# Optimization experiments

Hardware: AMD Instinct MI355X
Metric: run time of the kernel (lower is better)

The kernel has to match this reference:

```python
import jax, jax.numpy as jnp
import numpy as np

PLANES, RATIO = 512, 4
Q = PLANES // RATIO  # 128
B, H, W = 4, 128, 128


def _dw_stride2(x, k):
    # depthwise 3x3 stride-2 conv, NCHW, kernel [C,1,3,3]
    return jax.lax.conv_general_dilated(
        x, k, window_strides=(2, 2), padding=((1, 1), (1, 1)),
        feature_group_count=x.shape[1],
        dimension_numbers=('NCHW', 'OIHW', 'NCHW'))


def _upsample_bilinear_ac(x, out_h, out_w):
    # bilinear, align_corners=True (matches F.interpolate)
    n, c, h, w = x.shape
    def co(out, ins):
        s = (ins - 1) / (out - 1)
        pos = jnp.arange(out, dtype=jnp.float32) * jnp.float32(s)
        i0 = jnp.floor(pos).astype(jnp.int32)
        i1 = jnp.minimum(i0 + 1, ins - 1)
        return i0, i1, pos - i0.astype(jnp.float32)
    y0, y1, ty = co(out_h, h)
    x0, x1, tx = co(out_w, w)
    rows = x[:, :, y0, :] * (1 - ty)[None, None, :, None] + x[:, :, y1, :] * ty[None, None, :, None]
    return rows[:, :, :, x0] * (1 - tx) + rows[:, :, :, x1] * tx


def setup_inputs() -> dict:
    key = jax.random.key(0)
    ks = jax.random.split(key, 32)
    nrm = lambda k, s, sc=0.05: jax.random.normal(k, s, jnp.float32) * sc
    uni = lambda k, s: jax.random.uniform(k, s, jnp.float32, 0.5, 1.5)
    return {
        'feat': jax.random.normal(ks[0], (B, PLANES, H, W), jnp.float32),
        'w_phi': nrm(ks[1], (2 * Q, PLANES)),
        'bn_phi_s': uni(ks[2], (2 * Q,)), 'bn_phi_b': nrm(ks[3], (2 * Q,)),
        'w_theta': nrm(ks[4], (Q, PLANES)),
        'bn_theta_s': uni(ks[5], (Q,)), 'bn_theta_b': nrm(ks[6], (Q,)),
        'w_adj': nrm(ks[7], (Q, Q)),
        'bn_adj_s': uni(ks[8], (Q,)), 'bn_adj_b': nrm(ks[9], (Q,)),
        'w_wg': nrm(ks[10], (2 * Q, 2 * Q)),
        'bn_wg_s': uni(ks[11], (2 * Q,)), 'bn_wg_b': nrm(ks[12], (2 * Q,)),
        'w_conv3': nrm(ks[13], (PLANES, 2 * Q)),
        'bn3_s': uni(ks[14], (PLANES,)), 'bn3_b': nrm(ks[15], (PLANES,)),
        'w_local1': nrm(ks[16], (PLANES, 1, 3, 3), 0.2),
        'bnl1_s': uni(ks[17], (PLANES,)), 'bnl1_b': nrm(ks[18], (PLANES,)),
        'w_local2': nrm(ks[19], (PLANES, 1, 3, 3), 0.2),
        'bnl2_s': uni(ks[20], (PLANES,)), 'bnl2_b': nrm(ks[21], (PLANES,)),
        'w_local3': nrm(ks[22], (PLANES, 1, 3, 3), 0.2),
        'bnl3_s': uni(ks[23], (PLANES,)), 'bnl3_b': nrm(ks[24], (PLANES,)),
        'gamma': nrm(ks[25], (1,), 0.5),
        'w_final': nrm(ks[26], (PLANES, 2 * PLANES)),
        'bnf_s': uni(ks[27], (PLANES,)), 'bnf_b': nrm(ks[28], (PLANES,)),
    }


def reference(feat, w_phi, bn_phi_s, bn_phi_b, w_theta, bn_theta_s, bn_theta_b,
              w_adj, bn_adj_s, bn_adj_b, w_wg, bn_wg_s, bn_wg_b,
              w_conv3, bn3_s, bn3_b,
              w_local1, bnl1_s, bnl1_b, w_local2, bnl2_s, bnl2_b,
              w_local3, bnl3_s, bnl3_b, gamma, w_final, bnf_s, bnf_b):
    n, c, h, w = feat.shape
    bn2 = lambda x, s, b: x * s[None, :, None, None] + b[None, :, None, None]
    bn1 = lambda x, s, b: x * s[None, :, None] + b[None, :, None]
    conv1x1 = lambda x, wt: jnp.einsum('oc,nchw->nohw', wt, x)

    l = bn2(_dw_stride2(feat, w_local1), bnl1_s, bnl1_b)
    l = bn2(_dw_stride2(l, w_local2), bnl2_s, bnl2_b)
    l = bn2(_dw_stride2(l, w_local3), bnl3_s, bnl3_b)
    nl, cl, hl, wl = l.shape
    v = l.reshape(nl, cl, hl * wl)                      # [n,C,hw]
    energy = jnp.einsum('nck,ndk->ncd', v, v)           # [n,C,C]
    attn = jax.nn.softmax(jnp.max(energy, -1, keepdims=True) - energy, axis=-1)
    cam = jnp.einsum('ncd,ndk->nck', attn, v).reshape(nl, cl, hl, wl)
    l = gamma * cam + l
    local = _upsample_bilinear_ac(l, h, w)
    spatial_local_feat = feat * local + feat

    # ---- graph branch
    q = w_theta.shape[0]
    x_sqz = bn2(conv1x1(feat, w_phi), bn_phi_s, bn_phi_b).reshape(n, 2 * q, h * w)
    b_m = bn2(conv1x1(feat, w_theta), bn_theta_s, bn_theta_b).reshape(n, q, h * w)
    z_idt = jnp.einsum('nck,ndk->ncd', x_sqz, b_m)      # [n,2q,q]
    z = jnp.swapaxes(z_idt, 1, 2)                       # [n,q,2q]
    z = bn1(jnp.einsum('oi,nil->nol', w_adj, z), bn_adj_s, bn_adj_b)
    z = jnp.swapaxes(z, 1, 2) + z_idt                   # [n,2q,q]
    z = bn1(jnp.einsum('oi,nil->nol', w_wg, z), bn_wg_s, bn_wg_b)
    y = jnp.einsum('ncd,ndk->nck', z, b_m).reshape(n, 2 * q, h, w)
    y = bn2(conv1x1(y, w_conv3), bn3_s, bn3_b)
    g_out = jax.nn.relu(feat + y)

    out = bn2(conv1x1(jnp.concatenate([spatial_local_feat, g_out], axis=1), w_final), bnf_s, bnf_b)
    return out
```

## Files before the change

### kernel.cpp

```cpp
#include <hip/hip_runtime.h>
#include <hip/hip_bf16.h>
#include <cstddef>
#include <cstdint>

static constexpr int NB  = 4;
static constexpr int CH  = 512;
static constexpr int HH  = 128;
static constexpr int WWi = 128;
static constexpr int HW  = HH * WWi;
static constexpr int Qd  = 128;
static constexpr int Q2d = 256;

typedef __attribute__((ext_vector_type(8))) short bf8;
typedef __attribute__((ext_vector_type(4))) float f4;

__device__ __forceinline__ short f2bf(float x) {
  __hip_bfloat16 h = __float2bfloat16(x);
  short s; __builtin_memcpy(&s, &h, 2); return s;
}
__device__ __forceinline__ float bfs2f(short u) {
  union { unsigned int i; float f; } x;
  x.i = ((unsigned int)(unsigned short)u) << 16; return x.f;
}

__launch_bounds__(256)
__global__ void dw_conv_bn4(const float* __restrict__ in, float* __restrict__ out,
                            const float* __restrict__ wgt, const float* __restrict__ s,
                            const float* __restrict__ b, int Hi, int Wi, int Ho, int Wo4) {
  int idx = blockIdx.x * 256 + threadIdx.x;
  int q = idx % Wo4; int t = idx / Wo4;
  int ho = t % Ho; t /= Ho;
  int c = t % CH;
  const float* ip = in + (size_t)t * Hi * Wi;
  const float* wp = wgt + c * 9;
  float w[9];
#pragma unroll
  for (int k = 0; k < 9; k++) w[k] = wp[k];
  const int x0 = q * 8;
  float acc0 = 0.f, acc1 = 0.f, acc2 = 0.f, acc3 = 0.f;
#pragma unroll
  for (int kh = 0; kh < 3; kh++) {
    int y = ho * 2 - 1 + kh;
    if ((unsigned)y < (unsigned)Hi) {
      const float* row = ip + (size_t)y * Wi + x0;
      float4 v0 = *(const float4*)row;
      float4 v1 = *(const float4*)(row + 4);
      float left = (x0 > 0) ? row[-1] : 0.f;
      float xs[9] = {left, v0.x, v0.y, v0.z, v0.w, v1.x, v1.y, v1.z, v1.w};
      const float w0 = w[kh * 3 + 0], w1 = w[kh * 3 + 1], w2 = w[kh * 3 + 2];
      acc0 += w0 * xs[0] + w1 * xs[1] + w2 * xs[2];
      acc1 += w0 * xs[2] + w1 * xs[3] + w2 * xs[4];
      acc2 += w0 * xs[4] + w1 * xs[5] + w2 * xs[6];
      acc3 += w0 * xs[6] + w1 * xs[7] + w2 * xs[8];
    }
  }
  const float sc = s[c], bb = b[c];
  float4 o;
  o.x = acc0 * sc + bb; o.y = acc1 * sc + bb;
  o.z = acc2 * sc + bb; o.w = acc3 * sc + bb;
  *(float4*)(out + (size_t)idx * 4) = o;
}

__launch_bounds__(256)
__global__ void lrow_kernel(const float* __restrict__ lcam, float* __restrict__ lrow) {
  int idx = blockIdx.x * 256 + threadIdx.x;
  int wcol = idx & 127; int t = idx >> 7;
  int hy = t & 15; t >>= 4;
  float pos = wcol * (15.f / 127.f);
  int x0 = (int)pos; if (x0 > 15) x0 = 15;
  float tx = pos - x0;
  int x1 = x0 + 1; if (x1 > 15) x1 = 15;
  const float* lc = lcam + ((size_t)t * 16 + hy) * 16;
  lrow[idx] = lc[x0] * (1.f - tx) + lc[x1] * tx;
}

__launch_bounds__(256)
__global__ void cvt_f32_bf16(const float* __restrict__ in, short* __restrict__ out, int n4) {
  int i = blockIdx.x * 256 + threadIdx.x;
  if (i >= n4) return;
  float4 v = ((const float4*)in)[i];
  short tmp[4] = {f2bf(v.x), f2bf(v.y), f2bf(v.z), f2bf(v.w)};
  short4 o; __builtin_memcpy(&o, tmp, 8);
  ((short4*)out)[i] = o;
}

__device__ __forceinline__ int sls(int row, int slot) {
  return row * 64 + ((slot ^ (((row >> 1) ^ (row >> 3)) & 7)) << 3);
}

__device__ __forceinline__ void stg64_dma(const short* __restrict__ src, size_t stride,
                                          int kb, short* lds, int t) {
  const int lane = t & 63, w = t >> 6;
#pragma unroll
  for (int i2 = 0; i2 < 4; i2++) {
    int r0 = w * 32 + i2 * 8;
    int row = r0 + (lane >> 3);
    int sl = (lane & 7) ^ (((row >> 1) ^ (row >> 3)) & 7);
    const short* g = src + (size_t)row * stride + kb + sl * 8;
    short* l = lds + r0 * 64;
    __builtin_amdgcn_global_load_lds(
        (const __attribute__((address_space(1))) unsigned int*)g,
        (__attribute__((address_space(3))) unsigned int*)l, 16, 0, 0);
  }
}

__device__ __forceinline__ void stg64_b16(const short* __restrict__ src, size_t stride,
                                          int kb, short* lds, int t) {
#pragma unroll
  for (int i = 0; i < 4; i++) {
    int chunk = t + i * 256;
    int row = chunk >> 3, slot = chunk & 7;
    bf8 v = *(const bf8*)(src + (size_t)row * stride + kb + slot * 8);
    *(bf8*)(lds + sls(row, slot)) = v;
  }
}
__device__ __forceinline__ void stg64_f32(const float* __restrict__ src, size_t stride,
                                          int kb, short* lds, int t) {
#pragma unroll
  for (int i = 0; i < 4; i++) {
    int chunk = t + i * 256;
    int row = chunk >> 3, slot = chunk & 7;
    const float* sp = src + (size_t)row * stride + kb + slot * 8;
    float4 v0 = *(const float4*)sp, v1 = *(const float4*)(sp + 4);
    union { short s[8]; bf8 v; } u;
    u.s[0] = f2bf(v0.x); u.s[1] = f2bf(v0.y); u.s[2] = f2bf(v0.z); u.s[3] = f2bf(v0.w);
    u.s[4] = f2bf(v1.x); u.s[5] = f2bf(v1.y); u.s[6] = f2bf(v1.z); u.s[7] = f2bf(v1.w);
    *(bf8*)(lds + sls(row, slot)) = u.v;
  }
}
__device__ __forceinline__ void stg64_t32(const float* __restrict__ src, size_t sstride,
                                          int pb, short* lds, int t) {
#pragma unroll
  for (int i2 = 0; i2 < 4; i2++) {
    int chunk = t + i2 * 256;
    int c = (chunk >> 3) & 63;
    int p8 = ((chunk & 7) | ((chunk >> 6) & 8)) * 8;
    const float* fr = src + (size_t)c * sstride + pb + p8;
    float4 f0 = *(const float4*)fr, f1 = *(const float4*)(fr + 4);
    float fv[8];
    __builtin_memcpy(&fv[0], &f0, 16); __builtin_memcpy(&fv[4], &f1, 16);
    int slot = c >> 3, eidx = c & 7;
#pragma unroll
    for (int e = 0; e < 8; e++) {
      lds[sls(p8 + e, slot) + eidx] = f2bf(fv[e]);
    }
  }
}
__device__ __forceinline__ void stg64_t16(const short* __restrict__ src, size_t sstride,
                                          int pb, short* lds, int t) {
#pragma unroll
  for (int i2 = 0; i2 < 4; i2++) {
    int chunk = t + i2 * 256;
    int c = (chunk >> 3) & 63;
    int p8 = ((chunk & 7) | ((chunk >> 6) & 8)) * 8;
    bf8 v = *(const bf8*)(src + (size_t)c * sstride + pb + p8);
    int slot = c >> 3, eidx = c & 7;
#pragma unroll
    for (int e = 0; e < 8; e++) {
      lds[sls(p8 + e, slot) + eidx] = v[e];
    }
  }
}
__device__ __forceinline__ bf8 fragld64(const short* lds, int row, int kk, int lg) {
  return *(const bf8*)(lds + sls(row, kk * 4 + lg));
}

__launch_bounds__(256)
__global__ void slf_build_T(const float* __restrict__ feat, const float* __restrict__ lrw,
                            short* __restrict__ slfbT, int h0) {
  const int cb = blockIdx.x * 64;
  const int hh = blockIdx.y;
  const int n  = blockIdx.z;
  const int h  = hh + h0;
  const int t  = threadIdx.x;
  __shared__ __align__(16) short lT[8192];
  const float posy = h * (15.f / 127.f);
  int hy0 = (int)posy; if (hy0 > 15) hy0 = 15;
  int hy1 = hy0 + 1; if (hy1 > 15) hy1 = 15;
  const float tyv = posy - hy0;
#pragma unroll
  for (int i2 = 0; i2 < 4; i2++) {
    int chunk = t + i2 * 256;
    int c = (chunk >> 3) & 63;
    int w8 = ((chunk & 7) | ((chunk >> 6) & 8)) * 8;
    size_t cidx = (size_t)(n * CH) + cb + c;
    const float* fr = feat + cidx * HW + h * WWi + w8;
    const float* l0r = lrw + (cidx * 16 + hy0) * WWi + w8;
    const float* l1r = lrw + (cidx * 16 + hy1) * WWi + w8;
    float4 f0 = *(const float4*)fr, f1 = *(const float4*)(fr + 4);
    float4 a0 = *(const float4*)l0r, a1 = *(const float4*)(l0r + 4);
    float4 b0 = *(const float4*)l1r, b1 = *(const float4*)(l1r + 4);
    float fv[8], av[8], bv[8];
    __builtin_memcpy(&fv[0], &f0, 16); __builtin_memcpy(&fv[4], &f1, 16);
    __builtin_memcpy(&av[0], &a0, 16); __builtin_memcpy(&av[4], &a1, 16);
    __builtin_memcpy(&bv[0], &b0, 16); __builtin_memcpy(&bv[4], &b1, 16);
    int slot = c >> 3, eidx = c & 7;
#pragma unroll
    for (int e = 0; e < 8; e++) {
      float v = fv[e] * (1.f + av[e] + (bv[e] - av[e]) * tyv);
      lT[sls(w8 + e, slot) + eidx] = f2bf(v);
    }
  }
  __syncthreads();
#pragma unroll
  for (int i2 = 0; i2 < 4; i2++) {
    int chunk = t + i2 * 256;
    int w = chunk >> 3, slot = chunk & 7;
    bf8 v = *(const bf8*)(lT + sls(w, slot));
    *(bf8*)(slfbT + (((size_t)(n * 64) + hh) * WWi + w) * CH + cb + slot * 8) = v;
  }
}

__launch_bounds__(256)
__global__ void energy_mfma(const float* __restrict__ l3, float* __restrict__ energy) {
  const int c0 = blockIdx.x * 128;
  const int d0 = blockIdx.y * 128;
  const int n = blockIdx.z;
  const int t = threadIdx.x;
  const int lane16 = t & 15, lg = (t >> 4) & 3, wave = t >> 6;
  const int wm = (wave >> 1) * 64, wn = (wave & 1) * 64;
  __shared__ __align__(16) short lA[8192], lB[8192];
  const float* srcA = l3 + ((size_t)n * CH + c0) * 256;
  const float* srcB = l3 + ((size_t)n * CH + d0) * 256;
  f4 acc[4][4];
#pragma unroll
  for (int i = 0; i < 4; i++)
#pragma unroll
    for (int j = 0; j < 4; j++) acc[i][j] = (f4)0.f;
  for (int kb = 0; kb < 256; kb += 64) {
    stg64_f32(srcA, 256, kb, lA, t);
    stg64_f32(srcB, 256, kb, lB, t);
    __syncthreads();
#pragma unroll
    for (int kk = 0; kk < 2; kk++) {
      bf8 av[4], bv[4];
#pragma unroll
      for (int i = 0; i < 4; i++) av[i] = fragld64(lA, wm + i * 16 + lane16, kk, lg);
#pragma unroll
      for (int j = 0; j < 4; j++) bv[j] = fragld64(lB, wn + j * 16 + lane16, kk, lg);
#pragma unroll
      for (int i = 0; i < 4; i++)
#pragma unroll
        for (int j = 0; j < 4; j++)
          acc[i][j] = __builtin_amdgcn_mfma_f32_16x16x32_bf16(av[i], bv[j], acc[i][j], 0, 0, 0);
    }
    __syncthreads();
  }
#pragma unroll
  for (int i = 0; i < 4; i++)
#pragma unroll
    for (int j = 0; j < 4; j++) {
      int d = d0 + wn + j * 16 + lane16;
#pragma unroll
      for (int r = 0; r < 4; r++) {
        int c = c0 + wm + i * 16 + lg * 4 + r;
        energy[((size_t)n * CH + c) * CH + d] = acc[i][j][r];
      }
    }
}

__launch_bounds__(256)
__global__ void softmax_attn(float* __restrict__ energy) {
  float* row = energy + (size_t)blockIdx.x * CH;
  int t = threadIdx.x;
  __shared__ float red[256];
  float e0 = row[t], e1 = row[t + 256];
  red[t] = fminf(e0, e1);
  __syncthreads();
  for (int s = 128; s > 0; s >>= 1) {
    if (t < s) red[t] = fminf(red[t], red[t + s]);
    __syncthreads();
  }
  float emin = red[0];
  __syncthreads();
  float w0 = __expf(emin - e0), w1 = __expf(emin - e1);
  red[t] = w0 + w1;
  __syncthreads();
  for (int s = 128; s > 0; s >>= 1) {
    if (t < s) red[t] += red[t + s];
    __syncthreads();
  }
  float inv = 1.f / red[0];
  row[t] = w0 * inv;
  row[t + 256] = w1 * inv;
}

__launch_bounds__(256)
__global__ void cam_mfma(const float* __restrict__ attn, const float* __restrict__ l3,
                         const float* __restrict__ gamma, float* __restrict__ lcam) {
  const int pb = blockIdx.x * 128;
  const int mb = blockIdx.y * 128;
  const int n = blockIdx.z;
  const int t = threadIdx.x;
  const int lane16 = t & 15, lg = (t >> 4) & 3, wave = t >> 6;
  const int wm = (wave >> 1) * 64, wn = (wave & 1) * 64;
  __shared__ __align__(16) short lA[8192], lB[8192];
  const float* srcA = attn + ((size_t)n * CH + mb) * CH;
  const float gm = gamma[0];
  f4 acc[4][4];
#pragma unroll
  for (int i = 0; i < 4; i++)
#pragma unroll
    for (int j = 0; j < 4; j++) acc[i][j] = (f4)0.f;
  for (int kb = 0; kb < 512; kb += 64) {
    stg64_f32(srcA, CH, kb, lA, t);
    stg64_t32(l3 + ((size_t)n * CH + kb) * 256, 256, pb, lB, t);
    __syncthreads();
#pragma unroll
    for (int kk = 0; kk < 2; kk++) {
      bf8 av[4], bv[4];
#pragma unroll
      for (int i = 0; i < 4; i++) av[i] = fragld64(lA, wm + i * 16 + lane16, kk, lg);
#pragma unroll
      for (int j = 0; j < 4; j++) bv[j] = fragld64(lB, wn + j * 16 + lane16, kk, lg);
#pragma unroll
      for (int i = 0; i < 4; i++)
#pragma unroll
        for (int j = 0; j < 4; j++)
          acc[i][j] = __builtin_amdgcn_mfma_f32_16x16x32_bf16(av[i], bv[j], acc[i][j], 0, 0, 0);
    }
    __syncthreads();
  }
#pragma unroll
  for (int i = 0; i < 4; i++)
#pragma unroll
    for (int j = 0; j < 4; j++) {
      int p = pb + wn + j * 16 + lane16;
#pragma unroll
      for (int r = 0; r < 4; r++) {
        int c = mb + wm + i * 16 + lg * 4 + r;
        size_t idx = ((size_t)n * CH + c) * 256 + p;
        lcam[idx] = gm * acc[i][j][r] + l3[idx];
      }
    }
}

__launch_bounds__(256)
__global__ void theta_mfma2(const short* __restrict__ wthb, const float* __restrict__ feat,
                            const float* __restrict__ s, const float* __restrict__ b,
                            short* __restrict__ bmb) {
  const int pb = blockIdx.x * 128;
  const int n = blockIdx.y;
  const int t = threadIdx.x;
  const int lane16 = t & 15, lg = (t >> 4) & 3, wave = t >> 6;
  const int wm = (wave >> 1) * 64, wn = (wave & 1) * 64;
  __shared__ __align__(16) short lA[8192], lB[8192];
  f4 acc[4][4];
#pragma unroll
  for (int i = 0; i < 4; i++)
#pragma unroll
    for (int j = 0; j < 4; j++) acc[i][j] = (f4)0.f;
  for (int kb = 0; kb < 512; kb += 64) {
    stg64_dma(wthb, 512, kb, lA, t);
    stg64_t32(feat + ((size_t)(n * CH) + kb) * HW, HW, pb, lB, t);
    __syncthreads();
#pragma unroll
    for (int kk = 0; kk < 2; kk++) {
      bf8 av[4], bv[4];
#pragma unroll
      for (int i = 0; i < 4; i++) av[i] = fragld64(lA, wm + i * 16 + lane16, kk, lg);
#pragma unroll
      for (int j = 0; j < 4; j++) bv[j] = fragld64(lB, wn + j * 16 + lane16, kk, lg);
#pragma unroll
      for (int i = 0; i < 4; i++)
#pragma unroll
        for (int j = 0; j < 4; j++)
          acc[i][j] = __builtin_amdgcn_mfma_f32_16x16x32_bf16(av[i], bv[j], acc[i][j], 0, 0, 0);
    }
    __syncthreads();
  }
#pragma unroll
  for (int i = 0; i < 4; i++)
#pragma unroll
    for (int j = 0; j < 4; j++) {
      int p = pb + wn + j * 16 + lane16;
#pragma unroll
      for (int r = 0; r < 4; r++) {
        int d = wm + i * 16 + lg * 4 + r;
        bmb[((size_t)(n * Qd) + d) * HW + p] = f2bf(s[d] * acc[i][j][r] + b[d]);
      }
    }
}

__launch_bounds__(256)
__global__ void rowsum_bf(const short* __restrict__ bmb, float* __restrict__ rs) {
  int row = blockIdx.x;
  int t = threadIdx.x;
  const short* r = bmb + (size_t)row * HW;
  float a = 0.f;
  for (int p = t * 8; p < HW; p += 2048) {
    bf8 v = *(const bf8*)(r + p);
#pragma unroll
    for (int e = 0; e < 8; e++) a += bfs2f(v[e]);
  }
  __shared__ float red[256];
  red[t] = a;
  __syncthreads();
  for (int s = 128; s > 0; s >>= 1) {
    if (t < s) red[t] += red[t + s];
    __syncthreads();
  }
  if (t == 0) rs[row] = red[0];
}

__launch_bounds__(256)
__global__ void m1_mfma2(const float* __restrict__ feat, const short* __restrict__ bmb,
                         float* __restrict__ m1p) {
  const int c0 = blockIdx.x * 128;
  const int kc = blockIdx.y;
  const int n = blockIdx.z;
  const int t = threadIdx.x;
  const int lane16 = t & 15, lg = (t >> 4) & 3, wave = t >> 6;
  const int wm = (wave >> 1) * 64, wn = (wave & 1) * 64;
  __shared__ __align__(16) short lA[8192], lB[8192];
  const float* srcA = feat + ((size_t)(n * CH) + c0) * HW;
  const short* srcB = bmb + (size_t)(n * Qd) * HW;
  f4 acc[4][4];
#pragma unroll
  for (int i = 0; i < 4; i++)
#pragma unroll
    for (int j = 0; j < 4; j++) acc[i][j] = (f4)0.f;
  const int kend = kc * 512 + 512;
  for (int kb = kc * 512; kb < kend; kb += 64) {
    stg64_f32(srcA, HW, kb, lA, t);
    stg64_dma(srcB, HW, kb, lB, t);
    __syncthreads();
#pragma unroll
    for (int kk = 0; kk < 2; kk++) {
      bf8 av[4], bv[4];
#pragma unroll
      for (int i = 0; i < 4; i++) av[i] = fragld64(lA, wm + i * 16 + lane16, kk, lg);
#pragma unroll
      for (int j = 0; j < 4; j++) bv[j] = fragld64(lB, wn + j * 16 + lane16, kk, lg);
#pragma unroll
      for (int i = 0; i < 4; i++)
#pragma unroll
        for (int j = 0; j < 4; j++)
          acc[i][j] = __builtin_amdgcn_mfma_f32_16x16x32_bf16(av[i], bv[j], acc[i][j], 0, 0, 0);
    }
    __syncthreads();
  }
#pragma unroll
  for (int i = 0; i < 4; i++)
#pragma unroll
    for (int j = 0; j < 4; j++) {
      int d = wn + j * 16 + lane16;
#pragma unroll
      for (int r = 0; r < 4; r++) {
        int c = c0 + wm + i * 16 + lg * 4 + r;
        m1p[(((size_t)kc * NB + n) * CH + c) * Qd + d] = acc[i][j][r];
      }
    }
}

__launch_bounds__(256)
__global__ void m1_reduce(const float* __restrict__ m1p, float* __restrict__ m1) {
  int idx = blockIdx.x * 256 + threadIdx.x;
  float a = 0.f;
#pragma unroll
  for (int kc = 0; kc < 32; kc++) a += m1p[(size_t)kc * (NB * CH * Qd) + idx];
  m1[idx] = a;
}

__launch_bounds__(128)
__global__ void z3_fused(const float* __restrict__ m1, const float* __restrict__ wphi,
                         const float* __restrict__ sp, const float* __restrict__ bp,
                         const float* __restrict__ rs, const float* __restrict__ wadj,
                         const float* __restrict__ sa, const float* __restrict__ ba,
                         float* __restrict__ z3) {
  int n = blockIdx.y, c = blockIdx.x, d = threadIdx.x;
  __shared__ float wrow[512];
  __shared__ float zr[128];
  for (int i = d; i < 512; i += 128) wrow[i] = wphi[(size_t)c * 512 + i];
  __syncthreads();
  const float* mb = m1 + (size_t)n * CH * Qd;
  float acc = 0.f;
#pragma unroll 4
  for (int i = 0; i < 512; i++) acc += wrow[i] * mb[i * Qd + d];
  zr[d] = sp[c] * acc + bp[c] * rs[n * Qd + d];
  __syncthreads();
  const float* wr = wadj + (size_t)d * 128;
  float acc2 = 0.f;
#pragma unroll 4
  for (int i = 0; i < 128; i++) acc2 += wr[i] * zr[i];
  z3[((size_t)n * Q2d + c) * Qd + d] = sa[d] * acc2 + ba[d] + zr[d];
}

__launch_bounds__(128)
__global__ void z4_kernel(const float* __restrict__ z3, const float* __restrict__ wwg,
                          const float* __restrict__ sw, const float* __restrict__ bw,
                          float* __restrict__ z4) {
  int n = blockIdx.y, o = blockIdx.x, d = threadIdx.x;
  __shared__ float wrow[256];
  wrow[d] = wwg[(size_t)o * 256 + d];
  wrow[d + 128] = wwg[(size_t)o * 256 + 128 + d];
  __syncthreads();
  const float* zb = z3 + (size_t)n * Q2d * Qd;
  float acc = 0.f;
#pragma unroll 4
  for (int i = 0; i < 256; i++) acc += wrow[i] * zb[i * Qd + d];
  z4[((size_t)n * Q2d + o) * Qd + d] = sw[o] * acc + bw[o];
}

__launch_bounds__(128)
__global__ void wz_kernel(const float* __restrict__ z4, const float* __restrict__ wc3,
                          const float* __restrict__ s3, float* __restrict__ wz) {
  int n = blockIdx.y, o = blockIdx.x, d = threadIdx.x;
  __shared__ float wrow[256];
  wrow[d] = wc3[(size_t)o * 256 + d];
  wrow[d + 128] = wc3[(size_t)o * 256 + 128 + d];
  __syncthreads();
  const float* zb = z4 + (size_t)n * Q2d * Qd;
  float acc = 0.f;
#pragma unroll 4
  for (int i = 0; i < 256; i++) acc += wrow[i] * zb[i * Qd + d];
  wz[((size_t)n * CH + o) * Qd + d] = s3[o] * acc;
}

__launch_bounds__(256)
__global__ void ygout_mfma2(const float* __restrict__ wz, const short* __restrict__ bmb,
                            const float* __restrict__ feat, const float* __restrict__ b3,
                            short* __restrict__ goutT) {
  const int pb = blockIdx.x * 128;
  const int mb = blockIdx.y * 128;
  const int n = blockIdx.z;
  const int t = threadIdx.x;
  const int lane16 = t & 15, lg = (t >> 4) & 3, wave = t >> 6;
  const int wm = (wave >> 1) * 64, wn = (wave & 1) * 64;
  __shared__ __align__(16) short lA[8192], lB[8192];
  const float* srcA = wz + ((size_t)(n * CH) + mb) * Qd;
  f4 acc[4][4];
#pragma unroll
  for (int i = 0; i < 4; i++)
#pragma unroll
    for (int j = 0; j < 4; j++) acc[i][j] = (f4)0.f;
  for (int kb = 0; kb < 128; kb += 64) {
    stg64_f32(srcA, Qd, kb, lA, t);
    stg64_t16(bmb + ((size_t)(n * Qd) + kb) * HW, HW, pb, lB, t);
    __syncthreads();
#pragma unroll
    for (int kk = 0; kk < 2; kk++) {
      bf8 av[4], bv[4];
#pragma unroll
      for (int i = 0; i < 4; i++) av[i] = fragld64(lA, wm + i * 16 + lane16, kk, lg);
#pragma unroll
      for (int j = 0; j < 4; j++) bv[j] = fragld64(lB, wn + j * 16 + lane16, kk, lg);
#pragma unroll
      for (int i = 0; i < 4; i++)
#pragma unroll
        for (int j = 0; j < 4; j++)
          acc[i][j] = __builtin_amdgcn_mfma_f32_16x16x32_bf16(av[i], bv[j], acc[i][j], 0, 0, 0);
    }
    __syncthreads();
  }
#pragma unroll
  for (int i = 0; i < 4; i++)
#pragma unroll
    for (int j = 0; j < 4; j++) {
      int p = pb + wn + j * 16 + lane16;
      int c0 = mb + wm + i * 16 + lg * 4;
      union { short s[4]; short4 v; } u;
#pragma unroll
      for (int r = 0; r < 4; r++) {
        float g = feat[((size_t)(n * CH) + c0 + r) * HW + p] + acc[i][j][r] + b3[c0 + r];
        u.s[r] = f2bf(g > 0.f ? g : 0.f);
      }
      *(short4*)(goutT + ((size_t)(n * HW) + p) * CH + c0) = u.v;
    }
}

__launch_bounds__(256)
__global__ void final_mfma(const short* __restrict__ wfb, const short* __restrict__ slfbT,
                           const int h0, const short* __restrict__ goutT,
                           const float* __restrict__ fs, const float* __restrict__ fb,
                           float* __restrict__ out) {
  const int h = blockIdx.x + h0;
  const int pb = h * WWi;
  const int mb = blockIdx.y * 128;
  const int n = blockIdx.z;
  const int t = threadIdx.x;
  const int lane16 = t & 15, lg = (t >> 4) & 3, wave = t >> 6;
  const int wm = (wave >> 1) * 64, wn = (wave & 1) * 64;
  __shared__ __align__(16) short lA[8192], lB[8192];
  const short* slfRows = slfbT + ((size_t)(n * 64) + (h - h0)) * WWi * CH;
  const short* goutRows = goutT + ((size_t)(n * HW) + pb) * CH;
  f4 acc[4][4];
#pragma unroll
  for (int i = 0; i < 4; i++)
#pragma unroll
    for (int j = 0; j < 4; j++) acc[i][j] = (f4)0.f;

  for (int kb = 0; kb < 1024; kb += 64) {
    stg64_dma(wfb + (size_t)mb * 1024, 1024, kb, lA, t);
    if (kb < 512) {
      stg64_dma(slfRows, CH, kb, lB, t);
    } else {
      stg64_dma(goutRows, CH, kb - 512, lB, t);
    }
    __syncthreads();
#pragma unroll
    for (int kk = 0; kk < 2; kk++) {
      bf8 avf[4], bvf[4];
#pragma unroll
      for (int i = 0; i < 4; i++) avf[i] = fragld64(lA, wm + i * 16 + lane16, kk, lg);
#pragma unroll
      for (int j = 0; j < 4; j++) bvf[j] = fragld64(lB, wn + j * 16 + lane16, kk, lg);
#pragma unroll
      for (int i = 0; i < 4; i++)
#pragma unroll
        for (int j = 0; j < 4; j++)
          acc[i][j] = __builtin_amdgcn_mfma_f32_16x16x32_bf16(avf[i], bvf[j], acc[i][j], 0, 0, 0);
    }
    __syncthreads();
  }
#pragma unroll
  for (int i = 0; i < 4; i++)
#pragma unroll
    for (int j = 0; j < 4; j++) {
      int p = pb + wn + j * 16 + lane16;
#pragma unroll
      for (int r = 0; r < 4; r++) {
        int m = mb + wm + i * 16 + lg * 4 + r;
        out[((size_t)(n * CH) + m) * HW + p] = fs[m] * acc[i][j][r] + fb[m];
      }
    }
}

extern "C" void kernel_launch(void* const* d_in, const int* in_sizes, int n_in,
                              void* d_out, int out_size, void* d_ws, size_t ws_size,
                              hipStream_t stream) {
  (void)in_sizes; (void)n_in; (void)out_size; (void)ws_size;
  const float* feat      = (const float*)d_in[0];
  const float* w_phi     = (const float*)d_in[1];
  const float* bn_phi_s  = (const float*)d_in[2];
  const float* bn_phi_b  = (const float*)d_in[3];
  const float* w_theta   = (const float*)d_in[4];
  const float* bn_theta_s= (const float*)d_in[5];
  const float* bn_theta_b= (const float*)d_in[6];
  const float* w_adj     = (const float*)d_in[7];
  const float* bn_adj_s  = (const float*)d_in[8];
  const float* bn_adj_b  = (const float*)d_in[9];
  const float* w_wg      = (const float*)d_in[10];
  const float* bn_wg_s   = (const float*)d_in[11];
  const float* bn_wg_b   = (const float*)d_in[12];
  const float* w_conv3   = (const float*)d_in[13];
  const float* bn3_s     = (const float*)d_in[14];
  const float* bn3_b     = (const float*)d_in[15];
  const float* w_l1      = (const float*)d_in[16];
  const float* bnl1_s    = (const float*)d_in[17];
  const float* bnl1_b    = (const float*)d_in[18];
  const float* w_l2      = (const float*)d_in[19];
  const float* bnl2_s    = (const float*)d_in[20];
  const float* bnl2_b    = (const float*)d_in[21];
  const float* w_l3      = (const float*)d_in[22];
  const float* bnl3_s    = (const float*)d_in[23];
  const float* bnl3_b    = (const float*)d_in[24];
  const float* gamma     = (const float*)d_in[25];
  const float* w_final   = (const float*)d_in[26];
  const float* bnf_s     = (const float*)d_in[27];
  const float* bnf_b     = (const float*)d_in[28];

  float* out = (float*)d_out;
  float* l1 = out;
  float* l2 = l1 + (size_t)8388608;
  float* l3 = l2 + (size_t)2097152;
  short* wthb = (short*)(l3 + (size_t)524288);

  float* ws   = (float*)d_ws;
  float* lcam = ws;
  float* lrw  = lcam + (size_t)4 * 512 * 256;
  float* bm_region = lrw + (size_t)4 * 512 * 16 * 128;
  short* bmb  = (short*)bm_region;
  float* rsum = bm_region + (size_t)4 * 128 * 16384;
  float* M1   = rsum + 512;
  float* M1p_old = M1 + (size_t)4 * 512 * 128;
  float* zidt = M1p_old + (size_t)8 * 4 * 512 * 128;
  float* z3b  = zidt + (size_t)4 * 256 * 128;
  float* z4b  = z3b + (size_t)4 * 256 * 128;
  float* wzb  = z4b + (size_t)4 * 256 * 128;
  short* gout = (short*)(wzb + (size_t)4 * 512 * 128);
  short* wfb  = (short*)M1p_old;
  float* m1p  = (float*)gout;
  float* energy = (float*)M1p_old;
  short* slfb = (short*)bm_region;

  dw_conv_bn4<<<dim3(4 * 512 * 64 * 16 / 256), 256, 0, stream>>>(feat, l1, w_l1, bnl1_s, bnl1_b, 128, 128, 64, 16);
  dw_conv_bn4<<<dim3(4 * 512 * 32 * 8 / 256), 256, 0, stream>>>(l1, l2, w_l2, bnl2_s, bnl2_b, 64, 64, 32, 8);
  dw_conv_bn4<<<dim3(4 * 512 * 16 * 4 / 256), 256, 0, stream>>>(l2, l3, w_l3, bnl3_s, bnl3_b, 32, 32, 16, 4);
  energy_mfma<<<dim3(4, 4, 4), 256, 0, stream>>>(l3, energy);
  softmax_attn<<<dim3(4 * 512), 256, 0, stream>>>(energy);
  cam_mfma<<<dim3(2, 4, 4), 256, 0, stream>>>(energy, l3, gamma, lcam);
  lrow_kernel<<<dim3(4 * 512 * 16 * 128 / 256), 256, 0, stream>>>(lcam, lrw);

  cvt_f32_bf16<<<dim3(64), 256, 0, stream>>>(w_theta, wthb, 16384);
  theta_mfma2<<<dim3(128, 4), 256, 0, stream>>>(wthb, feat, bn_theta_s, bn_theta_b, bmb);
  rowsum_bf<<<dim3(512), 256, 0, stream>>>(bmb, rsum);
  m1_mfma2<<<dim3(4, 32, 4), 256, 0, stream>>>(feat, bmb, m1p);
  m1_reduce<<<dim3(1024), 256, 0, stream>>>(m1p, M1);
  z3_fused<<<dim3(256, 4), 128, 0, stream>>>(M1, w_phi, bn_phi_s, bn_phi_b, rsum, w_adj, bn_adj_s, bn_adj_b, z3b);
  z4_kernel<<<dim3(256, 4), 128, 0, stream>>>(z3b, w_wg, bn_wg_s, bn_wg_b, z4b);
  wz_kernel<<<dim3(512, 4), 128, 0, stream>>>(z4b, w_conv3, bn3_s, wzb);
  ygout_mfma2<<<dim3(128, 4, 4), 256, 0, stream>>>(wzb, bmb, feat, bn3_b, gout);

  cvt_f32_bf16<<<dim3(512), 256, 0, stream>>>(w_final, wfb, 131072);

  slf_build_T<<<dim3(8, 64, 4), 256, 0, stream>>>(feat, lrw, slfb, 0);
  final_mfma<<<dim3(64, 4, 4), 256, 0, stream>>>(wfb, slfb, 0, gout, bnf_s, bnf_b, out);
  slf_build_T<<<dim3(8, 64, 4), 256, 0, stream>>>(feat, lrw, slfb, 64);
  final_mfma<<<dim3(64, 4, 4), 256, 0, stream>>>(wfb, slfb, 64, gout, bnf_s, bnf_b, out);
}
```

Before: 454.4 us.

## Double-buffer B tiles in final GEMM to overlap DMA with MFMA

The final 1x1-conv GEMM now keeps two LDS buffers for the activation (B) tile and prefetches the next k-slice while the current one is consumed. Explicit vmcnt waits and raw s_barrier replace __syncthreads, so the weight tile load and the next B load can stay in flight during compute. This is meant to hide global-to-LDS latency in the final kernel. It costs extra LDS, which may reduce occupancy, and it relies on the vmcnt count matching the number of DMA instructions issued per stage.

```diff
diff --git a/kernel.cpp b/kernel.cpp
--- a/kernel.cpp
+++ b/kernel.cpp
@@ -581,37 +581,50 @@
   const int t = threadIdx.x;
   const int lane16 = t & 15, lg = (t >> 4) & 3, wave = t >> 6;
   const int wm = (wave >> 1) * 64, wn = (wave & 1) * 64;
-  __shared__ __align__(16) short lA[8192], lB[8192];
+  __shared__ __align__(16) short lA[8192], lB[2][8192];
   const short* slfRows = slfbT + ((size_t)(n * 64) + (h - h0)) * WWi * CH;
   const short* goutRows = goutT + ((size_t)(n * HW) + pb) * CH;
+  const short* wfRows = wfb + (size_t)mb * 1024;
   f4 acc[4][4];
 #pragma unroll
   for (int i = 0; i < 4; i++)
 #pragma unroll
     for (int j = 0; j < 4; j++) acc[i][j] = (f4)0.f;
 
-  for (int kb = 0; kb < 1024; kb += 64) {
-    stg64_dma(wfb + (size_t)mb * 1024, 1024, kb, lA, t);
-    if (kb < 512) {
-      stg64_dma(slfRows, CH, kb, lB, t);
+  auto stageB = [&](int s, int buf) {
+    if (s < 8) stg64_dma(slfRows, CH, s * 64, lB[buf], t);
+    else       stg64_dma(goutRows, CH, (s - 8) * 64, lB[buf], t);
+  };
+
+  stageB(0, 0);
+  int cur = 0;
+  for (int s = 0; s < 16; s++) {
+    stg64_dma(wfRows, 1024, s * 64, lA, t);
+    if (s + 1 < 16) stageB(s + 1, cur ^ 1);
+    if (s + 1 < 16) {
+      asm volatile("s_waitcnt vmcnt(4)" ::: "memory");
     } else {
-      stg64_dma(goutRows, CH, kb - 512, lB, t);
-    }
-    __syncthreads();
+      asm volatile("s_waitcnt vmcnt(0)" ::: "memory");
+    }
+    __builtin_amdgcn_sched_barrier(0);
+    __builtin_amdgcn_s_barrier();
+    __builtin_amdgcn_sched_barrier(0);
 #pragma unroll
     for (int kk = 0; kk < 2; kk++) {
       bf8 avf[4], bvf[4];
 #pragma unroll
       for (int i = 0; i < 4; i++) avf[i] = fragld64(lA, wm + i * 16 + lane16, kk, lg);
 #pragma unroll
-      for (int j = 0; j < 4; j++) bvf[j] = fragld64(lB, wn + j * 16 + lane16, kk, lg);
+      for (int j = 0; j < 4; j++) bvf[j] = fragld64(lB[cur], wn + j * 16 + lane16, kk, lg);
 #pragma unroll
       for (int i = 0; i < 4; i++)
 #pragma unroll
         for (int j = 0; j < 4; j++)
           acc[i][j] = __builtin_amdgcn_mfma_f32_16x16x32_bf16(avf[i], bvf[j], acc[i][j], 0, 0, 0);
     }
-    __syncthreads();
+    __builtin_amdgcn_sched_barrier(0);
+    __builtin_amdgcn_s_barrier();
+    cur ^= 1;
   }
 #pragma unroll
   for (int i = 0; i < 4; i++)
```

New measurement: 454.8 us. No clear change (+0.1%).
